# Performance work log

Hardware: AMD Instinct MI355X
Metric: run time of the kernel (lower is better)

The kernel has to match this reference:

```python
import jax, jax.numpy as jnp
import numpy as np

TOP_K = 2


def setup_inputs() -> dict:
    key = jax.random.key(0)
    k1, k2, k3, k4, k5 = jax.random.split(key, 5)
    B, S, H, I, E = 2, 2048, 1024, 1408, 8
    scale = 0.02
    return {
        "hidden_states": jax.random.normal(k1, (B, S, H), dtype=jnp.float32),
        "router_w": jax.random.normal(k2, (E, H), dtype=jnp.float32) * scale,
        "w_gate": jax.random.normal(k3, (E, I, H), dtype=jnp.float32) * scale,
        "w_up": jax.random.normal(k4, (E, I, H), dtype=jnp.float32) * scale,
        "w_down": jax.random.normal(k5, (E, H, I), dtype=jnp.float32) * scale,
    }


def reference(hidden_states, router_w, w_gate, w_up, w_down):
    B, S, H = hidden_states.shape
    E = router_w.shape[0]
    x = hidden_states.reshape(-1, H)  # [T, H]

    # Router: softmax over experts, take top-k, renormalize.
    probs = jax.nn.softmax(x @ router_w.T, axis=-1)          # [T, E]
    topk_w, topk_idx = jax.lax.top_k(probs, TOP_K)            # [T, k]
    topk_w = topk_w / (jnp.sum(topk_w, axis=-1, keepdims=True) + 1e-20)

    # Dense combine weights: zero for non-selected experts -> identical math
    # to the masked gather/scatter loop in the original module.
    combine = jnp.sum(
        topk_w[..., None] * jax.nn.one_hot(topk_idx, E, dtype=topk_w.dtype),
        axis=1,
    )  # [T, E]

    out = jnp.zeros_like(x)
    for e in range(E):  # small fixed expert count; unrolled under jit
        g = x @ w_gate[e].T                                   # [T, I]
        u = x @ w_up[e].T                                     # [T, I]
        ye = (jax.nn.silu(g) * u) @ w_down[e].T               # [T, H]
        out = out + combine[:, e:e + 1] * ye
    return out.reshape(B, S, H)
```

## Files before the change

### kernel.cpp

```cpp
#include <hip/hip_runtime.h>
#include <hip/hip_bf16.h>

#define T_TOK 4096
#define H_DIM 1024
#define I_DIM 1408
#define E_NUM 8
#define P_CAP 8192
#define G1_SLOTS 142
#define G2_SLOTS 71
#define G1_GRID (G1_SLOTS * 8)
#define G2_GRID (G2_SLOTS * 8)

typedef __bf16 bf16;
typedef __bf16 bf16x4 __attribute__((ext_vector_type(4)));
typedef __bf16 bf16x8 __attribute__((ext_vector_type(8)));
typedef float  f32x4  __attribute__((ext_vector_type(4)));

__device__ __forceinline__ void load_lds16(const void* g, void* l) {
  __builtin_amdgcn_global_load_lds((const __attribute__((address_space(1))) void*)g,
                                   (__attribute__((address_space(3))) void*)l, 16, 0, 0);
}

__global__ __launch_bounds__(256) void cast_all(const float* __restrict__ x,
                                                const float* __restrict__ wg,
                                                const float* __restrict__ wu,
                                                const float* __restrict__ wd,
                                                bf16* __restrict__ xb, bf16* __restrict__ wgb,
                                                bf16* __restrict__ wub, bf16* __restrict__ wdb) {
  int b = blockIdx.x;
  const float* s; bf16* d; int base;
  if (b < 4096)       { s = x;  d = xb;  base = b; }
  else if (b < 15360) { s = wg; d = wgb; base = b - 4096; }
  else if (b < 26624) { s = wu; d = wub; base = b - 15360; }
  else                { s = wd; d = wdb; base = b - 26624; }
  size_t i = ((size_t)base * 256 + threadIdx.x) * 4;
  float4 v = *(const float4*)(s + i);
  bf16x4 o;
  o.x = (bf16)v.x; o.y = (bf16)v.y; o.z = (bf16)v.z; o.w = (bf16)v.w;
  *(bf16x4*)(d + i) = o;
}

__global__ __launch_bounds__(256) void router_kernel(const float* __restrict__ x,
                                                     const float* __restrict__ rw,
                                                     int* __restrict__ tidx,
                                                     float* __restrict__ tw) {
  int t = blockIdx.x * 4 + (threadIdx.x >> 6);
  int lane = threadIdx.x & 63;
  const float4* xr  = (const float4*)(x + (size_t)t * H_DIM);
  const float4* rw4 = (const float4*)rw;
  float acc[E_NUM];
#pragma unroll
  for (int e = 0; e < E_NUM; ++e) acc[e] = 0.f;
  for (int c = lane; c < H_DIM / 4; c += 64) {
    float4 xv = xr[c];
#pragma unroll
    for (int e = 0; e < E_NUM; ++e) {
      float4 rv = rw4[e * (H_DIM / 4) + c];
      acc[e] += xv.x * rv.x + xv.y * rv.y + xv.z * rv.z + xv.w * rv.w;
    }
  }
#pragma unroll
  for (int e = 0; e < E_NUM; ++e)
    for (int s = 32; s > 0; s >>= 1) acc[e] += __shfl_down(acc[e], s, 64);
  if (lane == 0) {
    int a = 0;
#pragma unroll
    for (int e = 1; e < E_NUM; ++e) if (acc[e] > acc[a]) a = e;
    int b = (a == 0) ? 1 : 0;
#pragma unroll
    for (int e = 0; e < E_NUM; ++e) if (e != a && acc[e] > acc[b]) b = e;
    float pb = expf(acc[b] - acc[a]);
    float inv = 1.f / (1.f + pb);
    tidx[t * 2] = a; tidx[t * 2 + 1] = b;
    tw[t * 2] = inv; tw[t * 2 + 1] = pb * inv;
  }
}

__global__ __launch_bounds__(256) void bucket_kernel(const int* __restrict__ tidx,
                                                     int* __restrict__ pair_tok,
                                                     int* __restrict__ inv,
                                                     int* __restrict__ counts,
                                                     int* __restrict__ offsets,
                                                     int* __restrict__ sched1,
                                                     int* __restrict__ sched2) {
  __shared__ int sc[E_NUM], so[E_NUM];
  __shared__ int wcnt[4 * E_NUM];
  __shared__ int wbase[4 * E_NUM];
  const int tid = threadIdx.x, lane = tid & 63, wv = tid >> 6;

  int lc0 = 0, lc1 = 0, lc2 = 0, lc3 = 0, lc4 = 0, lc5 = 0, lc6 = 0, lc7 = 0;
  for (int base = wv * 64; base < P_CAP; base += 256) {
    int e = tidx[base + lane];
    lc0 += __popcll(__ballot(e == 0)); lc1 += __popcll(__ballot(e == 1));
    lc2 += __popcll(__ballot(e == 2)); lc3 += __popcll(__ballot(e == 3));
    lc4 += __popcll(__ballot(e == 4)); lc5 += __popcll(__ballot(e == 5));
    lc6 += __popcll(__ballot(e == 6)); lc7 += __popcll(__ballot(e == 7));
  }
  if (lane == 0) {
    wcnt[wv * 8 + 0] = lc0; wcnt[wv * 8 + 1] = lc1; wcnt[wv * 8 + 2] = lc2;
    wcnt[wv * 8 + 3] = lc3; wcnt[wv * 8 + 4] = lc4; wcnt[wv * 8 + 5] = lc5;
    wcnt[wv * 8 + 6] = lc6; wcnt[wv * 8 + 7] = lc7;
  }
  __syncthreads();

  if (tid == 0) {
    int run = 0;
    for (int e = 0; e < E_NUM; ++e) {
      int s = wcnt[e] + wcnt[8 + e] + wcnt[16 + e] + wcnt[24 + e];
      sc[e] = s; so[e] = run; run += s;
    }
  }
  __syncthreads();
  if (tid < 32) {
    int w = tid >> 3, e = tid & 7;
    int b = so[e];
    for (int ww = 0; ww < w; ++ww) b += wcnt[ww * 8 + e];
    wbase[tid] = b;
  }
  if (tid < E_NUM) { counts[tid] = sc[tid]; offsets[tid] = so[tid]; }
  __syncthreads();

  int wb0 = wbase[wv * 8 + 0], wb1 = wbase[wv * 8 + 1], wb2 = wbase[wv * 8 + 2],
      wb3 = wbase[wv * 8 + 3], wb4 = wbase[wv * 8 + 4], wb5 = wbase[wv * 8 + 5],
      wb6 = wbase[wv * 8 + 6], wb7 = wbase[wv * 8 + 7];
  const unsigned long long lt = (1ull << lane) - 1ull;
  for (int base = wv * 64; base < P_CAP; base += 256) {
    int p = base + lane;
    int e = tidx[p];
    int pos = 0;
    unsigned long long m;
    m = __ballot(e == 0); if (e == 0) pos = wb0 + __popcll(m & lt); wb0 += __popcll(m);
    m = __ballot(e == 1); if (e == 1) pos = wb1 + __popcll(m & lt); wb1 += __popcll(m);
    m = __ballot(e == 2); if (e == 2) pos = wb2 + __popcll(m & lt); wb2 += __popcll(m);
    m = __ballot(e == 3); if (e == 3) pos = wb3 + __popcll(m & lt); wb3 += __popcll(m);
    m = __ballot(e == 4); if (e == 4) pos = wb4 + __popcll(m & lt); wb4 += __popcll(m);
    m = __ballot(e == 5); if (e == 5) pos = wb5 + __popcll(m & lt); wb5 += __popcll(m);
    m = __ballot(e == 6); if (e == 6) pos = wb6 + __popcll(m & lt); wb6 += __popcll(m);
    m = __ballot(e == 7); if (e == 7) pos = wb7 + __popcll(m & lt); wb7 += __popcll(m);
    pair_tok[pos] = p >> 1;
    inv[p] = pos;
  }

  if (tid < 8) {
    const int k = tid;
    int q = 0;
    for (int c = k; c < 88; c += 8) {
      int e = c / 11, n0 = c % 11;
      int mb = (sc[e] + 127) >> 7;
      for (int m = 0; m < mb; ++m) { sched1[q * 8 + k] = (e << 16) | (m << 8) | n0; ++q; }
    }
    for (; q < G1_SLOTS; ++q) sched1[q * 8 + k] = -1;
    q = 0;
    for (int e = 0; e < E_NUM; ++e) {
      int mb = (sc[e] + 127) >> 7;
      for (int m = 0; m < mb; ++m) { sched2[q * 8 + k] = (e << 16) | (m << 8) | k; ++q; }
    }
    for (; q < G2_SLOTS; ++q) sched2[q * 8 + k] = -1;
  }
}

__global__ __launch_bounds__(256, 2)
void gemm1_kernel(const bf16* __restrict__ xb, const bf16* __restrict__ wgb,
                  const bf16* __restrict__ wub, const int* __restrict__ pair_tok,
                  const int* __restrict__ counts, const int* __restrict__ offsets,
                  const int* __restrict__ sched1, bf16* __restrict__ mid) {
  const int sv = sched1[blockIdx.x];
  if (sv < 0) return;
  const int e  = sv >> 16;
  const int m0 = ((sv >> 8) & 0xff) << 7;
  const int n0 = (sv & 0xff) << 7;
  const int cnt = counts[e];
  const int off = offsets[e];

  __shared__ bf16 As[128 * 64];
  __shared__ bf16 Bgs[128 * 64];
  __shared__ bf16 Bus[128 * 64];

  const int tid = threadIdx.x;
  const int wave = tid >> 6;
  const int lane = tid & 63;
  const int wm = (wave >> 1) << 6;
  const int wn = (wave & 1) << 6;

  const bf16* wg_e = wgb + (size_t)e * (I_DIM * H_DIM);
  const bf16* wu_e = wub + (size_t)e * (I_DIM * H_DIM);

  int arow[4], acs[4], atok[4];
#pragma unroll
  for (int j = 0; j < 4; ++j) {
    int seg = ((wave << 2) + j) * 64 + lane;
    int row = seg >> 3;
    arow[j] = row;
    acs[j]  = ((seg & 7) ^ (row & 7)) << 3;
    int gr = m0 + row;
    int cr = gr < cnt ? gr : cnt - 1;
    atok[j] = pair_tok[off + cr];
  }

  f32x4 accg[4][4], accu[4][4];
#pragma unroll
  for (int i = 0; i < 4; ++i)
#pragma unroll
    for (int j = 0; j < 4; ++j) {
      accg[i][j] = (f32x4){0.f, 0.f, 0.f, 0.f};
      accu[i][j] = (f32x4){0.f, 0.f, 0.f, 0.f};
    }

  const int lr = lane & 15;
  const int sw = lr & 7;
  const int qd = lane >> 4;

  for (int k0 = 0; k0 < H_DIM; k0 += 64) {
#pragma unroll
    for (int j = 0; j < 4; ++j) {
      int base = ((wave << 2) + j) << 9;
      load_lds16(xb + (size_t)atok[j] * H_DIM + k0 + acs[j], As + base);
      load_lds16(wg_e + (size_t)(n0 + arow[j]) * H_DIM + k0 + acs[j], Bgs + base);
      load_lds16(wu_e + (size_t)(n0 + arow[j]) * H_DIM + k0 + acs[j], Bus + base);
    }
    __syncthreads();
#pragma unroll
    for (int ks = 0; ks < 2; ++ks) {
      const int kc = (((ks << 2) + qd) ^ sw) << 3;
      bf16x8 a[4], bg[4], bu[4];
#pragma unroll
      for (int i = 0; i < 4; ++i)
        a[i] = *(const bf16x8*)(As + (wm + (i << 4) + lr) * 64 + kc);
#pragma unroll
      for (int j = 0; j < 4; ++j) {
        bg[j] = *(const bf16x8*)(Bgs + (wn + (j << 4) + lr) * 64 + kc);
        bu[j] = *(const bf16x8*)(Bus + (wn + (j << 4) + lr) * 64 + kc);
      }
#pragma unroll
      for (int i = 0; i < 4; ++i)
#pragma unroll
        for (int j = 0; j < 4; ++j) {
          accg[i][j] = __builtin_amdgcn_mfma_f32_16x16x32_bf16(a[i], bg[j], accg[i][j], 0, 0, 0);
          accu[i][j] = __builtin_amdgcn_mfma_f32_16x16x32_bf16(a[i], bu[j], accu[i][j], 0, 0, 0);
        }
    }
    __syncthreads();
  }

#pragma unroll
  for (int i = 0; i < 4; ++i) {
#pragma unroll
    for (int r = 0; r < 4; ++r) {
      int row = wm + (i << 4) + (qd << 2) + r;
      int gr = m0 + row;
      if (gr < cnt) {
        bf16* mrow = mid + (size_t)(off + gr) * I_DIM + n0 + wn;
#pragma unroll
        for (int j = 0; j < 4; ++j) {
          float g = accg[i][j][r], u = accu[i][j][r];
          float s = g / (1.f + __expf(-g));
          mrow[(j << 4) + lr] = (bf16)(s * u);
        }
      }
    }
  }
}

__global__ __launch_bounds__(256, 2)
void gemm2_kernel(const bf16* __restrict__ mid, const bf16* __restrict__ wdb,
                  const int* __restrict__ counts, const int* __restrict__ offsets,
                  const int* __restrict__ sched2, float* __restrict__ ybuf) {
  const int sv = sched2[blockIdx.x];
  if (sv < 0) return;
  const int e  = sv >> 16;
  const int m0 = ((sv >> 8) & 0xff) << 7;
  const int n0 = (sv & 0xff) << 7;
  const int cnt = counts[e];
  const int off = offsets[e];

  __shared__ bf16 As[128 * 64];
  __shared__ bf16 Bs[128 * 64];

  const int tid = threadIdx.x;
  const int wave = tid >> 6;
  const int lane = tid & 63;
  const int wm = (wave >> 1) << 6;
  const int wn = (wave & 1) << 6;

  const bf16* wd_e = wdb + (size_t)e * (H_DIM * I_DIM);

  int arow[4], acs[4];
  size_t apos[4];
#pragma unroll
  for (int j = 0; j < 4; ++j) {
    int seg = ((wave << 2) + j) * 64 + lane;
    int row = seg >> 3;
    arow[j] = row;
    acs[j]  = ((seg & 7) ^ (row & 7)) << 3;
    int gr = m0 + row;
    int cr = gr < cnt ? gr : cnt - 1;
    apos[j] = (size_t)(off + cr) * I_DIM + acs[j];
  }

  f32x4 acc[4][4];
#pragma unroll
  for (int i = 0; i < 4; ++i)
#pragma unroll
    for (int j = 0; j < 4; ++j) acc[i][j] = (f32x4){0.f, 0.f, 0.f, 0.f};

  const int lr = lane & 15;
  const int sw = lr & 7;
  const int qd = lane >> 4;

  for (int k0 = 0; k0 < I_DIM; k0 += 64) {
#pragma unroll
    for (int j = 0; j < 4; ++j) {
      int base = ((wave << 2) + j) << 9;
      load_lds16(mid + apos[j] + k0, As + base);
      load_lds16(wd_e + (size_t)(n0 + arow[j]) * I_DIM + k0 + acs[j], Bs + base);
    }
    __syncthreads();
#pragma unroll
    for (int ks = 0; ks < 2; ++ks) {
      const int kc = (((ks << 2) + qd) ^ sw) << 3;
      bf16x8 a[4], b[4];
#pragma unroll
      for (int i = 0; i < 4; ++i)
        a[i] = *(const bf16x8*)(As + (wm + (i << 4) + lr) * 64 + kc);
#pragma unroll
      for (int j = 0; j < 4; ++j)
        b[j] = *(const bf16x8*)(Bs + (wn + (j << 4) + lr) * 64 + kc);
#pragma unroll
      for (int i = 0; i < 4; ++i)
#pragma unroll
        for (int j = 0; j < 4; ++j)
          acc[i][j] = __builtin_amdgcn_mfma_f32_16x16x32_bf16(a[i], b[j], acc[i][j], 0, 0, 0);
    }
    __syncthreads();
  }

#pragma unroll
  for (int i = 0; i < 4; ++i) {
#pragma unroll
    for (int r = 0; r < 4; ++r) {
      int row = wm + (i << 4) + (qd << 2) + r;
      int gr = m0 + row;
      if (gr < cnt) {
        float* yrow = ybuf + (size_t)(off + gr) * H_DIM + n0 + wn;
#pragma unroll
        for (int j = 0; j < 4; ++j)
          yrow[(j << 4) + lr] = acc[i][j][r];
      }
    }
  }
}

__global__ __launch_bounds__(256) void combine_kernel(const float* __restrict__ ybuf,
                                                      const int* __restrict__ inv,
                                                      const float* __restrict__ tw,
                                                      float* __restrict__ out) {
  int t = blockIdx.x;
  int p0 = inv[2 * t], p1 = inv[2 * t + 1];
  float w0 = tw[2 * t], w1 = tw[2 * t + 1];
  int h = threadIdx.x * 4;
  float4 a = *(const float4*)(ybuf + (size_t)p0 * H_DIM + h);
  float4 b = *(const float4*)(ybuf + (size_t)p1 * H_DIM + h);
  float4 o;
  o.x = w0 * a.x + w1 * b.x;
  o.y = w0 * a.y + w1 * b.y;
  o.z = w0 * a.z + w1 * b.z;
  o.w = w0 * a.w + w1 * b.w;
  *(float4*)(out + (size_t)t * H_DIM + h) = o;
}

extern "C" void kernel_launch(void* const* d_in, const int* in_sizes, int n_in,
                              void* d_out, int out_size, void* d_ws, size_t ws_size,
                              hipStream_t stream) {
  const float* x  = (const float*)d_in[0];
  const float* rw = (const float*)d_in[1];
  const float* wg = (const float*)d_in[2];
  const float* wu = (const float*)d_in[3];
  const float* wd = (const float*)d_in[4];
  float* out = (float*)d_out;

  char* ws = (char*)d_ws;
  bf16*  xb      = (bf16*)(ws);
  bf16*  wgb     = (bf16*)(ws + 8388608);
  bf16*  wub     = (bf16*)(ws + 31457280);
  bf16*  wdb     = (bf16*)(ws + 54525952);
  bf16*  mid     = (bf16*)(ws + 77594624);
  float* ybuf    = (float*)(ws + 8388608);
  int*   tidx    = (int*)(ws + 100663296);
  float* tw      = (float*)(ws + 100696064);
  int*   ptok    = (int*)(ws + 100728832);
  int*   inv     = (int*)(ws + 100761600);
  int*   counts  = (int*)(ws + 100794368);
  int*   offsets = (int*)(ws + 100794400);
  int*   sched1  = (int*)(ws + 100794432);
  int*   sched2  = (int*)(ws + 100799232);

  cast_all<<<37888, 256, 0, stream>>>(x, wg, wu, wd, xb, wgb, wub, wdb);
  router_kernel<<<1024, 256, 0, stream>>>(x, rw, tidx, tw);
  bucket_kernel<<<1, 256, 0, stream>>>(tidx, ptok, inv, counts, offsets, sched1, sched2);
  gemm1_kernel<<<G1_GRID, 256, 0, stream>>>(xb, wgb, wub, ptok, counts, offsets, sched1, mid);
  gemm2_kernel<<<G2_GRID, 256, 0, stream>>>(mid, wdb, counts, offsets, sched2, ybuf);
  combine_kernel<<<T_TOK, 256, 0, stream>>>(ybuf, inv, tw, out);
}
```

Before: 320.3 us.

## Fuse fp32-to-bf16 casts into router and GEMM weight-tile loads

Removes the separate cast_all kernel. The activation cast now happens inside the router kernel, and the gemm1/gemm2 kernels read fp32 weights directly, converting them to bf16 in registers before writing the swizzled LDS tiles. This avoids a full read-fp32/write-bf16/re-read-bf16 pass over about 138 MB of weights. The cost is that each weight tile is re-read as fp32 (twice the bytes) by every M-block of an expert. The B loads also become synchronous register loads instead of async global_load_lds, and the workspace layout is repacked.

```diff
diff --git a/kernel.cpp b/kernel.cpp
--- a/kernel.cpp
+++ b/kernel.cpp
@@ -21,38 +21,24 @@
                                    (__attribute__((address_space(3))) void*)l, 16, 0, 0);
 }
 
-__global__ __launch_bounds__(256) void cast_all(const float* __restrict__ x,
-                                                const float* __restrict__ wg,
-                                                const float* __restrict__ wu,
-                                                const float* __restrict__ wd,
-                                                bf16* __restrict__ xb, bf16* __restrict__ wgb,
-                                                bf16* __restrict__ wub, bf16* __restrict__ wdb) {
-  int b = blockIdx.x;
-  const float* s; bf16* d; int base;
-  if (b < 4096)       { s = x;  d = xb;  base = b; }
-  else if (b < 15360) { s = wg; d = wgb; base = b - 4096; }
-  else if (b < 26624) { s = wu; d = wub; base = b - 15360; }
-  else                { s = wd; d = wdb; base = b - 26624; }
-  size_t i = ((size_t)base * 256 + threadIdx.x) * 4;
-  float4 v = *(const float4*)(s + i);
-  bf16x4 o;
-  o.x = (bf16)v.x; o.y = (bf16)v.y; o.z = (bf16)v.z; o.w = (bf16)v.w;
-  *(bf16x4*)(d + i) = o;
-}
-
 __global__ __launch_bounds__(256) void router_kernel(const float* __restrict__ x,
                                                      const float* __restrict__ rw,
                                                      int* __restrict__ tidx,
-                                                     float* __restrict__ tw) {
+                                                     float* __restrict__ tw,
+                                                     bf16* __restrict__ xb) {
   int t = blockIdx.x * 4 + (threadIdx.x >> 6);
   int lane = threadIdx.x & 63;
   const float4* xr  = (const float4*)(x + (size_t)t * H_DIM);
+  bf16* xbr = xb + (size_t)t * H_DIM;
   const float4* rw4 = (const float4*)rw;
   float acc[E_NUM];
 #pragma unroll
   for (int e = 0; e < E_NUM; ++e) acc[e] = 0.f;
   for (int c = lane; c < H_DIM / 4; c += 64) {
     float4 xv = xr[c];
+    bf16x4 o;
+    o.x = (bf16)xv.x; o.y = (bf16)xv.y; o.z = (bf16)xv.z; o.w = (bf16)xv.w;
+    *(bf16x4*)(xbr + c * 4) = o;
 #pragma unroll
     for (int e = 0; e < E_NUM; ++e) {
       float4 rv = rw4[e * (H_DIM / 4) + c];
@@ -160,8 +146,8 @@
 }
 
 __global__ __launch_bounds__(256, 2)
-void gemm1_kernel(const bf16* __restrict__ xb, const bf16* __restrict__ wgb,
-                  const bf16* __restrict__ wub, const int* __restrict__ pair_tok,
+void gemm1_kernel(const bf16* __restrict__ xb, const float* __restrict__ wg,
+                  const float* __restrict__ wu, const int* __restrict__ pair_tok,
                   const int* __restrict__ counts, const int* __restrict__ offsets,
                   const int* __restrict__ sched1, bf16* __restrict__ mid) {
   const int sv = sched1[blockIdx.x];
@@ -182,21 +168,25 @@
   const int wm = (wave >> 1) << 6;
   const int wn = (wave & 1) << 6;
 
-  const bf16* wg_e = wgb + (size_t)e * (I_DIM * H_DIM);
-  const bf16* wu_e = wub + (size_t)e * (I_DIM * H_DIM);
-
-  int arow[4], acs[4], atok[4];
+  const float* wg_e = wg + (size_t)e * (I_DIM * H_DIM);
+  const float* wu_e = wu + (size_t)e * (I_DIM * H_DIM);
+
+  int acs[4], atok[4];
 #pragma unroll
   for (int j = 0; j < 4; ++j) {
     int seg = ((wave << 2) + j) * 64 + lane;
     int row = seg >> 3;
-    arow[j] = row;
     acs[j]  = ((seg & 7) ^ (row & 7)) << 3;
     int gr = m0 + row;
     int cr = gr < cnt ? gr : cnt - 1;
     atok[j] = pair_tok[off + cr];
   }
 
+  const int brow_base = (wave << 2) + (lane >> 4);
+  const int bcol = (lane & 15) << 2;
+  const int bchunk = (lane & 15) >> 1;
+  const int bfrac = (lane & 1) << 2;
+
   f32x4 accg[4][4], accu[4][4];
 #pragma unroll
   for (int i = 0; i < 4; ++i)
@@ -215,8 +205,19 @@
     for (int j = 0; j < 4; ++j) {
       int base = ((wave << 2) + j) << 9;
       load_lds16(xb + (size_t)atok[j] * H_DIM + k0 + acs[j], As + base);
-      load_lds16(wg_e + (size_t)(n0 + arow[j]) * H_DIM + k0 + acs[j], Bgs + base);
-      load_lds16(wu_e + (size_t)(n0 + arow[j]) * H_DIM + k0 + acs[j], Bus + base);
+    }
+#pragma unroll
+    for (int i = 0; i < 8; ++i) {
+      int row = (i << 4) + brow_base;
+      const size_t gidx = (size_t)(n0 + row) * H_DIM + k0 + bcol;
+      float4 g = *(const float4*)(wg_e + gidx);
+      float4 u = *(const float4*)(wu_e + gidx);
+      int la = row * 64 + ((bchunk ^ (row & 7)) << 3) + bfrac;
+      bf16x4 gb, ub;
+      gb.x = (bf16)g.x; gb.y = (bf16)g.y; gb.z = (bf16)g.z; gb.w = (bf16)g.w;
+      ub.x = (bf16)u.x; ub.y = (bf16)u.y; ub.z = (bf16)u.z; ub.w = (bf16)u.w;
+      *(bf16x4*)(Bgs + la) = gb;
+      *(bf16x4*)(Bus + la) = ub;
     }
     __syncthreads();
 #pragma unroll
@@ -262,7 +263,7 @@
 }
 
 __global__ __launch_bounds__(256, 2)
-void gemm2_kernel(const bf16* __restrict__ mid, const bf16* __restrict__ wdb,
+void gemm2_kernel(const bf16* __restrict__ mid, const float* __restrict__ wd,
                   const int* __restrict__ counts, const int* __restrict__ offsets,
                   const int* __restrict__ sched2, float* __restrict__ ybuf) {
   const int sv = sched2[blockIdx.x];
@@ -282,21 +283,25 @@
   const int wm = (wave >> 1) << 6;
   const int wn = (wave & 1) << 6;
 
-  const bf16* wd_e = wdb + (size_t)e * (H_DIM * I_DIM);
-
-  int arow[4], acs[4];
+  const float* wd_e = wd + (size_t)e * (H_DIM * I_DIM);
+
+  int acs[4];
   size_t apos[4];
 #pragma unroll
   for (int j = 0; j < 4; ++j) {
     int seg = ((wave << 2) + j) * 64 + lane;
     int row = seg >> 3;
-    arow[j] = row;
     acs[j]  = ((seg & 7) ^ (row & 7)) << 3;
     int gr = m0 + row;
     int cr = gr < cnt ? gr : cnt - 1;
     apos[j] = (size_t)(off + cr) * I_DIM + acs[j];
   }
 
+  const int brow_base = (wave << 2) + (lane >> 4);
+  const int bcol = (lane & 15) << 2;
+  const int bchunk = (lane & 15) >> 1;
+  const int bfrac = (lane & 1) << 2;
+
   f32x4 acc[4][4];
 #pragma unroll
   for (int i = 0; i < 4; ++i)
@@ -312,7 +317,15 @@
     for (int j = 0; j < 4; ++j) {
       int base = ((wave << 2) + j) << 9;
       load_lds16(mid + apos[j] + k0, As + base);
-      load_lds16(wd_e + (size_t)(n0 + arow[j]) * I_DIM + k0 + acs[j], Bs + base);
+    }
+#pragma unroll
+    for (int i = 0; i < 8; ++i) {
+      int row = (i << 4) + brow_base;
+      float4 v = *(const float4*)(wd_e + (size_t)(n0 + row) * I_DIM + k0 + bcol);
+      int la = row * 64 + ((bchunk ^ (row & 7)) << 3) + bfrac;
+      bf16x4 vb;
+      vb.x = (bf16)v.x; vb.y = (bf16)v.y; vb.z = (bf16)v.z; vb.w = (bf16)v.w;
+      *(bf16x4*)(Bs + la) = vb;
     }
     __syncthreads();
 #pragma unroll
@@ -380,24 +393,20 @@
 
   char* ws = (char*)d_ws;
   bf16*  xb      = (bf16*)(ws);
-  bf16*  wgb     = (bf16*)(ws + 8388608);
-  bf16*  wub     = (bf16*)(ws + 31457280);
-  bf16*  wdb     = (bf16*)(ws + 54525952);
-  bf16*  mid     = (bf16*)(ws + 77594624);
-  float* ybuf    = (float*)(ws + 8388608);
-  int*   tidx    = (int*)(ws + 100663296);
-  float* tw      = (float*)(ws + 100696064);
-  int*   ptok    = (int*)(ws + 100728832);
-  int*   inv     = (int*)(ws + 100761600);
-  int*   counts  = (int*)(ws + 100794368);
-  int*   offsets = (int*)(ws + 100794400);
-  int*   sched1  = (int*)(ws + 100794432);
-  int*   sched2  = (int*)(ws + 100799232);
-
-  cast_all<<<37888, 256, 0, stream>>>(x, wg, wu, wd, xb, wgb, wub, wdb);
-  router_kernel<<<1024, 256, 0, stream>>>(x, rw, tidx, tw);
+  bf16*  mid     = (bf16*)(ws + 8388608);
+  float* ybuf    = (float*)(ws + 31457280);
+  int*   tidx    = (int*)(ws + 65011712);
+  float* tw      = (float*)(ws + 65044480);
+  int*   ptok    = (int*)(ws + 65077248);
+  int*   inv     = (int*)(ws + 65110016);
+  int*   counts  = (int*)(ws + 65142784);
+  int*   offsets = (int*)(ws + 65142816);
+  int*   sched1  = (int*)(ws + 65142848);
+  int*   sched2  = (int*)(ws + 65147648);
+
+  router_kernel<<<1024, 256, 0, stream>>>(x, rw, tidx, tw, xb);
   bucket_kernel<<<1, 256, 0, stream>>>(tidx, ptok, inv, counts, offsets, sched1, sched2);
-  gemm1_kernel<<<G1_GRID, 256, 0, stream>>>(xb, wgb, wub, ptok, counts, offsets, sched1, mid);
-  gemm2_kernel<<<G2_GRID, 256, 0, stream>>>(mid, wdb, counts, offsets, sched2, ybuf);
+  gemm1_kernel<<<G1_GRID, 256, 0, stream>>>(xb, wg, wu, ptok, counts, offsets, sched1, mid);
+  gemm2_kernel<<<G2_GRID, 256, 0, stream>>>(mid, wd, counts, offsets, sched2, ybuf);
   combine_kernel<<<T_TOK, 256, 0, stream>>>(ybuf, inv, tw, out);
 }
```

Result: slower. 391.9 us (+22.4%).
